# Kernel optimization log

Hardware: AMD Instinct MI355X
Metric: run time of the kernel (lower is better)

Reference implementation:

```python
import jax, jax.numpy as jnp
import numpy as np

N_HEAD = 8
LN_EPS = 1e-5


def layernorm(x, g, b):
    m = x.mean(-1, keepdims=True)
    var = x.var(-1, keepdims=True)
    return (x - m) / jnp.sqrt(var + LN_EPS) * g + b


def mha(xq, xkv, key_pad, w, b, wo, bo):
    # w: [3, D, D] (q,k,v proj), key_pad: [B, Nk] bool, True = ignore
    B, Nq, D = xq.shape
    H, dh = N_HEAD, D // N_HEAD
    q = (xq @ w[0] + b[0]).reshape(B, Nq, H, dh)
    k = (xkv @ w[1] + b[1]).reshape(B, -1, H, dh)
    v = (xkv @ w[2] + b[2]).reshape(B, -1, H, dh)
    s = jnp.einsum('bqhd,bkhd->bhqk', q, k) * (1.0 / np.float32(np.sqrt(dh)))
    s = jnp.where(key_pad[:, None, None, :], jnp.float32(-1e9), s)
    a = jax.nn.softmax(s, axis=-1)
    o = jnp.einsum('bhqk,bkhd->bqhd', a, v).reshape(B, Nq, D)
    return o @ wo + bo


def coattn_layer(v, q, v_pad, q_pad, aw, ab, awo, abo, lg, lb, fw1, fb1, fw2, fb2):
    # self-attention + residual + LN
    v_a = layernorm(v + mha(v, v, v_pad, aw[0], ab[0], awo[0], abo[0]), lg[0], lb[0])
    q_a = layernorm(q + mha(q, q, q_pad, aw[1], ab[1], awo[1], abo[1]), lg[1], lb[1])
    # cross attention: note qv_attn consumes OUTPUT of vq_attn (as in original)
    vq_out = mha(v_a, q_a, q_pad, aw[2], ab[2], awo[2], abo[2])
    qv_out = mha(q_a, vq_out, v_pad, aw[3], ab[3], awo[3], abo[3])
    v = layernorm(v + vq_out, lg[2], lb[2])
    q = layernorm(q + qv_out, lg[3], lb[3])
    # FFN (fc -> relu -> fc), residual + LN
    v = layernorm(v + (jax.nn.relu(v @ fw1[0] + fb1[0]) @ fw2[0] + fb2[0]), lg[4], lb[4])
    q = layernorm(q + (jax.nn.relu(q @ fw1[1] + fb1[1]) @ fw2[1] + fb2[1]), lg[5], lb[5])
    return v, q


def setup_inputs() -> dict:
    key = jax.random.key(0)
    B, NV, NQ, D, L = 8, 512, 512, 512, 4
    DF = 4 * D
    ks = jax.random.split(key, 12)
    sd = 0.02
    inp = {}
    inp['v'] = jax.random.normal(ks[0], (B, NV, D), jnp.float32)
    inp['q'] = jax.random.normal(ks[1], (B, NQ, D), jnp.float32)
    vm = jax.random.randint(ks[2], (B, NV), 0, 2, jnp.int32)
    qm = jax.random.randint(ks[3], (B, NQ), 0, 2, jnp.int32)
    inp['v_mask'] = vm.at[:, 0].set(1)  # ensure >=1 valid token per row
    inp['q_mask'] = qm.at[:, 0].set(1)
    inp['attn_w'] = sd * jax.random.normal(ks[4], (L, 4, 3, D, D), jnp.float32)
    inp['attn_b'] = jnp.zeros((L, 4, 3, D), jnp.float32)
    inp['attn_wo'] = sd * jax.random.normal(ks[5], (L, 4, D, D), jnp.float32)
    inp['attn_bo'] = jnp.zeros((L, 4, D), jnp.float32)
    inp['ln_g'] = jnp.ones((L, 6, D), jnp.float32)
    inp['ln_b'] = jnp.zeros((L, 6, D), jnp.float32)
    inp['ffn_w1'] = sd * jax.random.normal(ks[6], (L, 2, D, DF), jnp.float32)
    inp['ffn_b1'] = jnp.zeros((L, 2, DF), jnp.float32)
    inp['ffn_w2'] = sd * jax.random.normal(ks[7], (L, 2, DF, D), jnp.float32)
    inp['ffn_b2'] = jnp.zeros((L, 2, D), jnp.float32)
    inp['att_w'] = sd * jax.random.normal(ks[8], (D,), jnp.float32)
    inp['att_b'] = jnp.zeros((), jnp.float32)
    return inp


def reference(v, q, attn_w, attn_b, attn_wo, attn_bo, ln_g, ln_b,
              ffn_w1, ffn_b1, ffn_w2, ffn_b2, att_w, att_b, v_mask, q_mask):
    v_pad = v_mask == 0  # True = pad (original: ~v_mask.bool())
    q_pad = q_mask == 0
    L = attn_w.shape[0]
    for i in range(L):
        v, q = coattn_layer(v, q, v_pad, q_pad,
                            attn_w[i], attn_b[i], attn_wo[i], attn_bo[i],
                            ln_g[i], ln_b[i],
                            ffn_w1[i], ffn_b1[i], ffn_w2[i], ffn_b2[i])
    # att_net(v_i * q_j) is a bilinear form: sum_k v_bvk * q_bqk * w_k + bias
    s = jnp.einsum('bvk,bqk,k->bvq', v, q, att_w) + att_b
    cross_mask = v_pad[:, :, None] | q_pad[:, None, :]
    s = jnp.where(cross_mask, jnp.float32(-1e9), s)
    att_maps = jax.nn.softmax(s, axis=-1)
    v_num, q_num = v.shape[1], q.shape[1]
    seq_scale = 1.0 / np.float32(np.sqrt(v_num * q_num))
    return jnp.einsum('bvk,bvq,bqk->bk', v, att_maps, q) * seq_scale
```

## Files before the change

### kernel.cpp

```cpp
#include <hip/hip_runtime.h>
#include <hip/hip_bf16.h>

typedef __hip_bfloat16 bf16;
typedef __attribute__((ext_vector_type(8))) short short8;
typedef __attribute__((ext_vector_type(4))) short short4v;
typedef __attribute__((ext_vector_type(4))) float f32x4;

#define AS1 __attribute__((address_space(1)))
#define AS3 __attribute__((address_space(3)))

#define B_  8
#define N_  512
#define D_  512
#define H_  8
#define DH_ 64
#define DF_ 2048
#define L_  4

static __device__ __forceinline__ short bfbits(float x) {
  bf16 t = __float2bfloat16(x);
  return *reinterpret_cast<short*>(&t);
}

__global__ __launch_bounds__(256) void k_prep2(const float* __restrict__ a,
                                               float* __restrict__ fa, bf16* __restrict__ ba,
                                               const float* __restrict__ bsrc,
                                               float* __restrict__ fb, bf16* __restrict__ bb,
                                               int n4) {
  int g = blockIdx.x * 256 + threadIdx.x;
  const float* s; float* f; bf16* o; long idx;
  if (g < n4) { s = a;    f = fa; o = ba; idx = (long)g * 4; }
  else        { s = bsrc; f = fb; o = bb; idx = (long)(g - n4) * 4; }
  float4 v = *(const float4*)(s + idx);
  *(float4*)(f + idx) = v;
  bf16 ov[4] = { __float2bfloat16(v.x), __float2bfloat16(v.y),
                 __float2bfloat16(v.z), __float2bfloat16(v.w) };
  *(short4v*)&o[idx] = *(const short4v*)ov;
}

__global__ __launch_bounds__(256) void k_wt(const float* __restrict__ aw_l,
                                            const float* __restrict__ awo_l,
                                            const float* __restrict__ fw1_l,
                                            const float* __restrict__ fw2_l,
                                            bf16* __restrict__ WT)
{
  __shared__ float Ls[32][33];
  int bx = blockIdx.x;
  const float* src; bf16* dst; int R, C, tr, tc;
  if (bx < 4096) {
    int id = bx >> 8, t = bx & 255;
    int m = id >> 2, part = id & 3;
    src = (part < 3) ? (aw_l + ((long)m * 3 + part) * D_ * D_)
                     : (awo_l + (long)m * D_ * D_);
    dst = WT + (long)id * 262144; R = 512; C = 512; tr = t >> 4; tc = t & 15;
  } else if (bx < 6144) {
    int q = bx - 4096; int id = q >> 10; int t = q & 1023;
    src = fw1_l + (long)id * D_ * DF_; dst = WT + 4194304 + (long)id * 1048576;
    R = 512; C = 2048; tr = t >> 6; tc = t & 63;
  } else {
    int q = bx - 6144; int id = q >> 10; int t = q & 1023;
    src = fw2_l + (long)id * DF_ * D_; dst = WT + 6291456 + (long)id * 1048576;
    R = 2048; C = 512; tr = t >> 4; tc = t & 15;
  }
  int t = threadIdx.x;
  int lr = t >> 3, lc0 = (t & 7) * 4;
  float4 v = *(const float4*)(src + (long)(tr * 32 + lr) * C + tc * 32 + lc0);
  Ls[lr][lc0] = v.x; Ls[lr][lc0 + 1] = v.y; Ls[lr][lc0 + 2] = v.z; Ls[lr][lc0 + 3] = v.w;
  __syncthreads();
  bf16 ov[4];
#pragma unroll
  for (int j = 0; j < 4; ++j) ov[j] = __float2bfloat16(Ls[lc0 + j][lr]);
  *(short4v*)&dst[(long)(tc * 32 + lr) * R + tr * 32 + lc0] = *(const short4v*)ov;
}

template<int BN>
__global__ __launch_bounds__(256, 2) void k_mfma(
    const bf16* __restrict__ A, const bf16* __restrict__ A2,
    long aS, long aB, long aH, int lda,
    const bf16* __restrict__ Bm, long bS, long bB, long bH, int ldb,
    const float* __restrict__ bias, long biasS, float scale, int relu,
    float* __restrict__ Cf, long cfS, long cfB, long cfH, int ldcf,
    bf16* __restrict__ Cb, long cbS, long cbB, long cbH, int ldcb,
    int kLen, int Hh, int zPerS, int mode, int kSplit, long pStride)
{
  constexpr int MI = (BN == 128) ? 4 : 2;
  constexpr int NI = 4;
  __shared__ short As[2 * 128 * 32];
  __shared__ short Bs[2 * BN * 32];
  int tid = threadIdx.x;
  int w = tid >> 6, lane = tid & 63;
  int z = blockIdx.z;
  int kk = 0;
  if (kSplit > 1) { kk = z % kSplit; z /= kSplit; }
  int s = z / zPerS; int zz = z - s * zPerS;
  int zb = zz / Hh, zh = zz - zb * Hh;
  int row0 = blockIdx.y * 128;
  int col0 = blockIdx.x * BN;
  const bf16* Asel = (mode == 1 && col0 >= 512) ? A2 : A;
  const bf16* Ab = Asel + s * aS + zb * aB + zh * aH + (long)kk * kLen;
  const bf16* Bb = Bm + s * bS + zb * bB + zh * bH + (long)kk * kLen;
  int rw = (BN == 128) ? ((w >> 1) * 64) : (w * 32);
  int cw = (BN == 128) ? ((w & 1) * 64) : 0;
  int quad = lane >> 4, l16 = lane & 15;

  f32x4 acc[MI][NI];
#pragma unroll
  for (int i = 0; i < MI; ++i)
#pragma unroll
    for (int j = 0; j < NI; ++j) acc[i][j] = {0.f, 0.f, 0.f, 0.f};

  for (int k0 = 0; k0 < kLen; k0 += 64) {
#pragma unroll
    for (int hf = 0; hf < 2; ++hf) {
#pragma unroll
      for (int i = 0; i < 2; ++i) {
        int o = i * 4096 + w * 1024 + lane * 16;
        int r = o >> 6;
        const bf16* g = Ab + (long)(row0 + r) * lda + k0 + hf * 32 + ((o & 63) >> 1);
        char* lp = (char*)As + hf * 8192 + i * 4096 + w * 1024;
        __builtin_amdgcn_global_load_lds((const AS1 void*)g, (AS3 void*)lp, 16, 0, 0);
      }
      constexpr int BI = (BN == 128) ? 2 : 1;
#pragma unroll
      for (int i = 0; i < BI; ++i) {
        int o = i * 4096 + w * 1024 + lane * 16;
        int r = o >> 6;
        const bf16* g = Bb + (long)(col0 + r) * ldb + k0 + hf * 32 + ((o & 63) >> 1);
        char* lp = (char*)Bs + hf * (BN * 64) + i * 4096 + w * 1024;
        __builtin_amdgcn_global_load_lds((const AS1 void*)g, (AS3 void*)lp, 16, 0, 0);
      }
    }
    __syncthreads();
#pragma unroll
    for (int hf = 0; hf < 2; ++hf) {
      short8 af[MI], bfr[NI];
#pragma unroll
      for (int mi = 0; mi < MI; ++mi)
        af[mi] = *(const short8*)&As[hf * 4096 + (rw + mi * 16 + l16) * 32 + quad * 8];
#pragma unroll
      for (int ni = 0; ni < NI; ++ni)
        bfr[ni] = *(const short8*)&Bs[hf * (BN * 32) + (cw + ni * 16 + l16) * 32 + quad * 8];
#pragma unroll
      for (int mi = 0; mi < MI; ++mi)
#pragma unroll
        for (int ni = 0; ni < NI; ++ni)
          acc[mi][ni] = __builtin_amdgcn_mfma_f32_16x16x32_bf16(af[mi], bfr[ni], acc[mi][ni], 0, 0, 0);
    }
    __syncthreads();
  }

  const float* bp = (bias && kk == 0) ? bias + s * biasS : nullptr;
#pragma unroll
  for (int mi = 0; mi < MI; ++mi)
#pragma unroll
    for (int ni = 0; ni < NI; ++ni) {
      int cg = col0 + cw + ni * 16 + l16;
      float bv = bp ? bp[cg] : 0.0f;
#pragma unroll
      for (int r = 0; r < 4; ++r) {
        int rg = row0 + rw + mi * 16 + quad * 4 + r;
        float v = acc[mi][ni][r] * scale + bv;
        if (relu) v = fmaxf(v, 0.0f);
        if (mode == 1) {
          bf16* base = Cb + s * cbS;
          if (cg < 512) base[(long)rg * 512 + cg] = __float2bfloat16(v);
          else if (cg < 1024) base[2097152 + (long)rg * 512 + (cg - 512)] = __float2bfloat16(v);
          else {
            int c2 = cg - 1024;
            base[4194304 + ((long)((rg >> 9) * 8 + (c2 >> 6)) * 64 + (c2 & 63)) * 512 + (rg & 511)]
                = __float2bfloat16(v);
          }
        } else {
          if (Cf) Cf[s * cfS + (long)kk * pStride + zb * cfB + zh * cfH + (long)rg * ldcf + cg] = v;
          if (Cb) Cb[s * cbS + zb * cbB + zh * cbH + (long)rg * ldcb + cg] = __float2bfloat16(v);
        }
      }
    }
}

__global__ __launch_bounds__(256, 2) void k_flash(
    const bf16* __restrict__ QKV, long sStride,
    const int* __restrict__ km0, const int* __restrict__ km1, float scale)
{
  __shared__ short Ks[2 * 128 * 32];
  __shared__ short Vs[4 * 64 * 32];
  __shared__ short Ps[4 * 64 * 32];
  int tid = threadIdx.x, w = tid >> 6, lane = tid & 63;
  int quad = lane >> 4, l16 = lane & 15;
  int s = blockIdx.z;
  const bf16* base = QKV + s * sStride;
  int bh = blockIdx.y, b = bh >> 3, h = bh & 7;
  int qt = blockIdx.x;
  const int* km = (s ? km1 : km0) + (b << 9);
  const bf16* Kg = base + 2097152;
  const bf16* Vt = base + 4194304;
  bf16* Og = (bf16*)base;

  int qrow = (b << 9) + (qt << 6) + (w << 4) + l16;
  short8 qf[2];
  qf[0] = *(const short8*)&base[(long)qrow * 512 + h * 64 + quad * 8];
  qf[1] = *(const short8*)&base[(long)qrow * 512 + h * 64 + 32 + quad * 8];

  float m_[4], l_[4];
  f32x4 acc_o[4];
#pragma unroll
  for (int r = 0; r < 4; ++r) { m_[r] = -3e38f; l_[r] = 0.f; }
#pragma unroll
  for (int ni = 0; ni < 4; ++ni) acc_o[ni] = {0.f, 0.f, 0.f, 0.f};

  for (int kt = 0; kt < 4; ++kt) {
    __syncthreads();
#pragma unroll
    for (int i = 0; i < 4; ++i) {
      int o = i * 4096 + w * 1024 + lane * 16;
      int kc = o >> 13, rem = o & 8191;
      int n = rem >> 6, cb = rem & 63;
      const bf16* g = Kg + ((long)((b << 9) + kt * 128 + n) << 9) + h * 64 + kc * 32 + (cb >> 1);
      char* lp = (char*)Ks + i * 4096 + w * 1024;
      __builtin_amdgcn_global_load_lds((const AS1 void*)g, (AS3 void*)lp, 16, 0, 0);
    }
#pragma unroll
    for (int i = 0; i < 4; ++i) {
      int o = i * 4096 + w * 1024 + lane * 16;
      int kc = o >> 12, rem = o & 4095;
      int d = rem >> 6, cb = rem & 63;
      const bf16* g = Vt + ((long)((bh << 6) + d) << 9) + kt * 128 + kc * 32 + (cb >> 1);
      char* lp = (char*)Vs + i * 4096 + w * 1024;
      __builtin_amdgcn_global_load_lds((const AS1 void*)g, (AS3 void*)lp, 16, 0, 0);
    }
    __syncthreads();
    f32x4 sa[8];
#pragma unroll
    for (int ni = 0; ni < 8; ++ni) sa[ni] = {0.f, 0.f, 0.f, 0.f};
    __builtin_amdgcn_s_setprio(1);
#pragma unroll
    for (int kc = 0; kc < 2; ++kc)
#pragma unroll
      for (int ni = 0; ni < 8; ++ni) {
        short8 bfrag = *(const short8*)&Ks[kc * 4096 + (ni * 16 + l16) * 32 + quad * 8];
        sa[ni] = __builtin_amdgcn_mfma_f32_16x16x32_bf16(qf[kc], bfrag, sa[ni], 0, 0, 0);
      }
    __builtin_amdgcn_s_setprio(0);
    float sv[8][4];
#pragma unroll
    for (int ni = 0; ni < 8; ++ni) {
      int kmv = km[kt * 128 + ni * 16 + l16];
#pragma unroll
      for (int r = 0; r < 4; ++r)
        sv[ni][r] = kmv ? sa[ni][r] * scale : -1e9f;
    }
#pragma unroll
    for (int r = 0; r < 4; ++r) {
      float rmax = sv[0][r];
#pragma unroll
      for (int ni = 1; ni < 8; ++ni) rmax = fmaxf(rmax, sv[ni][r]);
#pragma unroll
      for (int o = 1; o < 16; o <<= 1) rmax = fmaxf(rmax, __shfl_xor(rmax, o, 64));
      float newm = fmaxf(m_[r], rmax);
      float alpha = __expf(m_[r] - newm);
      float psum = 0.f;
#pragma unroll
      for (int ni = 0; ni < 8; ++ni) {
        float p = __expf(sv[ni][r] - newm);
        sv[ni][r] = p; psum += p;
      }
#pragma unroll
      for (int o = 1; o < 16; o <<= 1) psum += __shfl_xor(psum, o, 64);
      l_[r] = l_[r] * alpha + psum;
      m_[r] = newm;
#pragma unroll
      for (int ni = 0; ni < 4; ++ni) acc_o[ni][r] *= alpha;
    }
#pragma unroll
    for (int ni = 0; ni < 8; ++ni) {
      int j = ni * 16 + l16;
      short* pp = &Ps[(j >> 5) * 2048 + (w * 16 + quad * 4) * 32 + (j & 31)];
#pragma unroll
      for (int r = 0; r < 4; ++r) pp[r * 32] = bfbits(sv[ni][r]);
    }
    __builtin_amdgcn_s_setprio(1);
#pragma unroll
    for (int kcp = 0; kcp < 4; ++kcp) {
      short8 af = *(const short8*)&Ps[kcp * 2048 + (w * 16 + l16) * 32 + quad * 8];
#pragma unroll
      for (int ni = 0; ni < 4; ++ni) {
        short8 bfrag = *(const short8*)&Vs[kcp * 2048 + (ni * 16 + l16) * 32 + quad * 8];
        acc_o[ni] = __builtin_amdgcn_mfma_f32_16x16x32_bf16(af, bfrag, acc_o[ni], 0, 0, 0);
      }
    }
    __builtin_amdgcn_s_setprio(0);
  }
  float linv[4];
#pragma unroll
  for (int r = 0; r < 4; ++r) linv[r] = 1.0f / l_[r];
#pragma unroll
  for (int ni = 0; ni < 4; ++ni)
#pragma unroll
    for (int r = 0; r < 4; ++r) {
      long row = (b << 9) + (qt << 6) + (w << 4) + quad * 4 + r;
      Og[row * 512 + h * 64 + ni * 16 + l16] = __float2bfloat16(acc_o[ni][r] * linv[r]);
    }
}

__global__ __launch_bounds__(256) void k_ln2(
    const float* x0, const float* g0, const float* b0, float* yf0, bf16* yb0,
    const float* x1, const float* g1, const float* b1, float* yf1, bf16* yb1,
    const float* __restrict__ P, long pstr)
{
  int t = threadIdx.x;
  int rh = t >> 7;
  long row = (long)blockIdx.x * 2 + rh;
  int sel = row >= 4096;
  long r = row & 4095;
  const float* x  = sel ? x1 : x0;
  const float* g  = sel ? g1 : g0;
  const float* bb = sel ? b1 : b0;
  float* yf = sel ? yf1 : yf0;
  bf16*  yb = sel ? yb1 : yb0;
  int c = (t & 127) * 4;
  const float* xr = x + r * D_ + c;
  const float* ra = P + (sel ? 2 : 0) * pstr + r * D_ + c;
  const float* rb = ra + pstr;
  float4 xv = *(const float4*)xr;
  float4 av = *(const float4*)ra;
  float4 bv = *(const float4*)rb;
  float4 v = { xv.x + av.x + bv.x, xv.y + av.y + bv.y,
               xv.z + av.z + bv.z, xv.w + av.w + bv.w };
  float s  = v.x + v.y + v.z + v.w;
  float ss = v.x * v.x + v.y * v.y + v.z * v.z + v.w * v.w;
#pragma unroll
  for (int o = 32; o > 0; o >>= 1) {
    s  += __shfl_down(s, o, 64);
    ss += __shfl_down(ss, o, 64);
  }
  __shared__ float rs[4];
  __shared__ float rss[4];
  int lane = t & 63, wid = t >> 6;
  if (lane == 0) { rs[wid] = s; rss[wid] = ss; }
  __syncthreads();
  s  = rs[rh * 2]  + rs[rh * 2 + 1];
  ss = rss[rh * 2] + rss[rh * 2 + 1];
  float mean = s * (1.0f / D_);
  float var = ss * (1.0f / D_) - mean * mean;
  float rstd = rsqrtf(var + 1e-5f);
  float4 gg = *(const float4*)(g + c);
  float4 b4 = *(const float4*)(bb + c);
  float4 o4 = { (v.x - mean) * rstd * gg.x + b4.x,
                (v.y - mean) * rstd * gg.y + b4.y,
                (v.z - mean) * rstd * gg.z + b4.z,
                (v.w - mean) * rstd * gg.w + b4.w };
  if (yf) *(float4*)(yf + r * D_ + c) = o4;
  if (yb) {
    bf16 ov[4] = { __float2bfloat16(o4.x), __float2bfloat16(o4.y),
                   __float2bfloat16(o4.z), __float2bfloat16(o4.w) };
    *(short4v*)&yb[r * D_ + c] = *(const short4v*)ov;
  }
}

__global__ __launch_bounds__(256) void k_sum2bf(const float* __restrict__ a,
                                                const float* __restrict__ b,
                                                bf16* __restrict__ o)
{
  int i = (blockIdx.x * 256 + threadIdx.x) * 4;
  float4 va = *(const float4*)(a + i);
  float4 vb = *(const float4*)(b + i);
  bf16 ov[4] = { __float2bfloat16(va.x + vb.x), __float2bfloat16(va.y + vb.y),
                 __float2bfloat16(va.z + vb.z), __float2bfloat16(va.w + vb.w) };
  *(short4v*)&o[i] = *(const short4v*)ov;
}

__global__ __launch_bounds__(256) void k_softmax_x(float* __restrict__ S,
                                                   const int* __restrict__ vm,
                                                   const int* __restrict__ qm)
{
  int wrow = blockIdx.x * 4 + (threadIdx.x >> 6);
  int lane = threadIdx.x & 63;
  int b = wrow >> 9, i = wrow & 511;
  bool rowpad = (vm[(b << 9) + i] == 0);
  float* p = S + (long)wrow * 512;
  const int* qb = qm + (b << 9);
  int j0 = lane * 8;
  float4 a0 = *(const float4*)(p + j0);
  float4 a1 = *(const float4*)(p + j0 + 4);
  int4 m0 = *(const int4*)(qb + j0);
  int4 m1 = *(const int4*)(qb + j0 + 4);
  float v[8];
  v[0] = (rowpad || !m0.x) ? -1e9f : a0.x; v[1] = (rowpad || !m0.y) ? -1e9f : a0.y;
  v[2] = (rowpad || !m0.z) ? -1e9f : a0.z; v[3] = (rowpad || !m0.w) ? -1e9f : a0.w;
  v[4] = (rowpad || !m1.x) ? -1e9f : a1.x; v[5] = (rowpad || !m1.y) ? -1e9f : a1.y;
  v[6] = (rowpad || !m1.z) ? -1e9f : a1.z; v[7] = (rowpad || !m1.w) ? -1e9f : a1.w;
  float mx = v[0];
#pragma unroll
  for (int u = 1; u < 8; ++u) mx = fmaxf(mx, v[u]);
#pragma unroll
  for (int o = 1; o < 64; o <<= 1) mx = fmaxf(mx, __shfl_xor(mx, o, 64));
  float e[8], sum = 0.f;
#pragma unroll
  for (int u = 0; u < 8; ++u) { e[u] = __expf(v[u] - mx); sum += e[u]; }
#pragma unroll
  for (int o = 1; o < 64; o <<= 1) sum += __shfl_xor(sum, o, 64);
  float inv = 1.0f / sum;
  bf16 ob[8];
#pragma unroll
  for (int u = 0; u < 8; ++u) ob[u] = __float2bfloat16(e[u] * inv);
  bf16* pb = (bf16*)p;
  *(short8*)&pb[j0] = *(const short8*)ob;
}

__global__ __launch_bounds__(256) void k_vwqt(const float* __restrict__ V,
                                              const float* __restrict__ Q,
                                              const float* __restrict__ w,
                                              bf16* __restrict__ Vw, bf16* __restrict__ Qt)
{
  __shared__ float Ls[32][33];
  int bx = blockIdx.x, t = threadIdx.x;
  if (bx < 2048) {
    int i = bx * 1024 + t * 4;
    float4 v = *(const float4*)(V + i);
    int k = i & 511;
    bf16 o[4] = { __float2bfloat16(v.x * w[k]),     __float2bfloat16(v.y * w[k + 1]),
                  __float2bfloat16(v.z * w[k + 2]), __float2bfloat16(v.w * w[k + 3]) };
    *(short4v*)&Vw[i] = *(const short4v*)o;
  } else {
    int q = bx - 2048; int b = q >> 8; int tq = q & 255;
    int tr = tq >> 4, tc = tq & 15;
    const float* Qb = Q + (long)b * 262144;
    bf16* Qtb = Qt + (long)b * 262144;
    int lr = t >> 3, lc0 = (t & 7) * 4;
    float4 v = *(const float4*)(Qb + (long)(tr * 32 + lr) * 512 + tc * 32 + lc0);
    Ls[lr][lc0] = v.x; Ls[lr][lc0 + 1] = v.y; Ls[lr][lc0 + 2] = v.z; Ls[lr][lc0 + 3] = v.w;
    __syncthreads();
    bf16 ov[4];
#pragma unroll
    for (int j = 0; j < 4; ++j) ov[j] = __float2bfloat16(Ls[lc0 + j][lr]);
    *(short4v*)&Qtb[(long)(tc * 32 + lr) * 512 + tr * 32 + lc0] = *(const short4v*)ov;
  }
}

__global__ __launch_bounds__(256) void k_final_part(
    const float* __restrict__ V, const float* __restrict__ QT, float* __restrict__ Pf)
{
  int bx = blockIdx.x;
  int b = bx >> 5, rem = bx & 31;
  int kc = rem >> 4, is = rem & 15;
  int k = (kc << 8) + threadIdx.x;
  const float* Vb = V  + (long)b * N_ * D_ + (long)(is * 32) * D_ + k;
  const float* Tb = QT + (long)b * N_ * D_ + (long)(is * 32) * D_ + k;
  float acc = 0.0f;
#pragma unroll 8
  for (int i = 0; i < 32; ++i) acc += Vb[(long)i * D_] * Tb[(long)i * D_];
  Pf[bx * 256 + threadIdx.x] = acc;
}

__global__ __launch_bounds__(256) void k_fred(const float* __restrict__ Pf,
                                              float* __restrict__ out)
{
  int b = blockIdx.x >> 1, kc = blockIdx.x & 1;
  int k = (kc << 8) + threadIdx.x;
  float s = 0.0f;
#pragma unroll
  for (int is = 0; is < 16; ++is)
    s += Pf[(((b << 5) | (kc << 4) | is) << 8) + threadIdx.x];
  out[b * D_ + k] = s * (1.0f / 512.0f);
}

extern "C" void kernel_launch(void* const* d_in, const int* in_sizes, int n_in,
                              void* d_out, int out_size, void* d_ws, size_t ws_size,
                              hipStream_t stream)
{
  const float* in_v   = (const float*)d_in[0];
  const float* in_q   = (const float*)d_in[1];
  const int*   v_mask = (const int*)  d_in[2];
  const int*   q_mask = (const int*)  d_in[3];
  const float* aw  = (const float*)d_in[4];
  const float* ab  = (const float*)d_in[5];
  const float* awo = (const float*)d_in[6];
  const float* abo = (const float*)d_in[7];
  const float* lg  = (const float*)d_in[8];
  const float* lb  = (const float*)d_in[9];
  const float* fw1 = (const float*)d_in[10];
  const float* fb1 = (const float*)d_in[11];
  const float* fw2 = (const float*)d_in[12];
  const float* fb2 = (const float*)d_in[13];
  const float* atw = (const float*)d_in[14];
  const float* atb = (const float*)d_in[15];
  float* out = (float*)d_out;
  (void)atb;

  const int SZ = B_ * N_ * D_;
  char* wsb = (char*)d_ws;
  const long MB = 1024L * 1024;
  float* Vcur   = (float*)(wsb + 0 * MB);
  float* Qcur   = (float*)(wsb + 8 * MB);
  float* P0     = (float*)(wsb + 16 * MB);
  const long PSZ = 2097152;
  bf16*  WT     = (bf16*) (wsb + 48 * MB);
  bf16*  Vcur_b = (bf16*) (wsb + 64 * MB);
  bf16*  Qcur_b = (bf16*) (wsb + 68 * MB);
  bf16*  VA_b   = (bf16*) (wsb + 72 * MB);
  bf16*  QA_b   = (bf16*) (wsb + 76 * MB);
  bf16*  VQ_b   = (bf16*) (wsb + 80 * MB);
  bf16*  QKV0   = (bf16*) (wsb + 84 * MB);
  bf16*  Hid    = (bf16*) (wsb + 108 * MB);
  float* Sf     = P0;
  bf16*  Vw_b   = (bf16*) (wsb + 24 * MB);
  bf16*  Qt_b   = (bf16*) (wsb + 28 * MB);
  float* Tfin   = (float*)(wsb + 32 * MB);
  float* Pf     = (float*)(wsb + 41 * MB);

  const long ZBIG = 1000000;

  k_prep2<<<4096, 256, 0, stream>>>(in_v, Vcur, Vcur_b, in_q, Qcur, Qcur_b, SZ / 4);

  for (int l = 0; l < L_; ++l) {
    const float* lgl = lg + (long)l * 6 * D_;
    const float* lbl = lb + (long)l * 6 * D_;
    k_wt<<<8192, 256, 0, stream>>>(aw + (long)l * 12 * 262144,
                                   awo + (long)l * 4 * 262144,
                                   fw1 + (long)l * 2 * 1048576,
                                   fw2 + (long)l * 2 * 1048576, WT);
    k_mfma<128><<<dim3(12, 32, 2), 256, 0, stream>>>(
        Vcur_b, Vcur_b, 2097152, 0, 0, 512,
        WT, 1048576, 0, 0, 512,
        ab + (long)l * 4 * 1536, 1536, 1.f, 0,
        nullptr, 0, 0, 0, 0, QKV0, 6291456, 0, 0, 0,
        512, 1, 1, 1, 1, 0);
    k_flash<<<dim3(8, 64, 2), 256, 0, stream>>>(QKV0, 6291456, v_mask, q_mask, 0.125f);
    k_mfma<128><<<dim3(4, 32, 4), 256, 0, stream>>>(
        QKV0, QKV0, 6291456, 0, 0, 512,
        WT + 3 * 262144, 1048576, 0, 0, 512,
        abo + (long)l * 4 * 512, 512, 1.f, 0,
        P0, 2 * PSZ, 0, 0, 512, nullptr, 0, 0, 0, 0,
        256, 1, 1, 0, 2, PSZ);
    k_ln2<<<4096, 256, 0, stream>>>(Vcur, lgl + 0 * D_, lbl + 0 * D_, nullptr, VA_b,
                                    Qcur, lgl + 1 * D_, lbl + 1 * D_, nullptr, QA_b,
                                    P0, PSZ);
    k_mfma<128><<<dim3(12, 32, 1), 256, 0, stream>>>(
        VA_b, QA_b, 0, 0, 0, 512,
        WT + 2 * 1048576, 0, 0, 0, 512,
        ab + (long)(l * 4 + 2) * 1536, 0, 1.f, 0,
        nullptr, 0, 0, 0, 0, QKV0, 0, 0, 0, 0,
        512, 1, 1, 1, 1, 0);
    k_flash<<<dim3(8, 64, 1), 256, 0, stream>>>(QKV0, 0, q_mask, q_mask, 0.125f);
    k_mfma<64><<<dim3(8, 32, 2), 256, 0, stream>>>(
        QKV0, QKV0, 0, 0, 0, 512,
        WT + (2 * 4 + 3) * 262144, 0, 0, 0, 512,
        abo + (long)(l * 4 + 2) * 512, 0, 1.f, 0,
        P0, 0, 0, 0, 512, nullptr, 0, 0, 0, 0,
        256, 1, 1, 0, 2, PSZ);
    k_sum2bf<<<2048, 256, 0, stream>>>(P0, P0 + PSZ, VQ_b);
    k_mfma<128><<<dim3(12, 32, 1), 256, 0, stream>>>(
        QA_b, VQ_b, 0, 0, 0, 512,
        WT + 3 * 1048576, 0, 0, 0, 512,
        ab + (long)(l * 4 + 3) * 1536, 0, 1.f, 0,
        nullptr, 0, 0, 0, 0, QKV0, 0, 0, 0, 0,
        512, 1, 1, 1, 1, 0);
    k_flash<<<dim3(8, 64, 1), 256, 0, stream>>>(QKV0, 0, v_mask, v_mask, 0.125f);
    k_mfma<64><<<dim3(8, 32, 2), 256, 0, stream>>>(
        QKV0, QKV0, 0, 0, 0, 512,
        WT + (3 * 4 + 3) * 262144, 0, 0, 0, 512,
        abo + (long)(l * 4 + 3) * 512, 0, 1.f, 0,
        P0 + 2 * PSZ, 0, 0, 0, 512, nullptr, 0, 0, 0, 0,
        256, 1, 1, 0, 2, PSZ);
    k_ln2<<<4096, 256, 0, stream>>>(Vcur, lgl + 2 * D_, lbl + 2 * D_, Vcur, Vcur_b,
                                    Qcur, lgl + 3 * D_, lbl + 3 * D_, Qcur, Qcur_b,
                                    P0, PSZ);
    k_mfma<128><<<dim3(16, 32, 2), 256, 0, stream>>>(
        Vcur_b, Vcur_b, 2097152, 0, 0, 512,
        WT + 4194304, 1048576, 0, 0, 512,
        fb1 + (long)l * 2 * 2048, 2048, 1.f, 1,
        nullptr, 0, 0, 0, 0, Hid, 8388608, 0, 0, 2048,
        512, 1, 1, 0, 1, 0);
    k_mfma<128><<<dim3(4, 32, 4), 256, 0, stream>>>(
        Hid, Hid, 8388608, 0, 0, 2048,
        WT + 6291456, 1048576, 0, 0, 2048,
        fb2 + (long)l * 2 * 512, 512, 1.f, 0,
        P0, 2 * PSZ, 0, 0, 512, nullptr, 0, 0, 0, 0,
        1024, 1, 1, 0, 2, PSZ);
    k_ln2<<<4096, 256, 0, stream>>>(Vcur, lgl + 4 * D_, lbl + 4 * D_, Vcur, Vcur_b,
                                    Qcur, lgl + 5 * D_, lbl + 5 * D_, Qcur, Qcur_b,
                                    P0, PSZ);
  }

  k_vwqt<<<4096, 256, 0, stream>>>(Vcur, Qcur, atw, Vw_b, Qt_b);
  k_mfma<128><<<dim3(4, 4, 8), 256, 0, stream>>>(
      Vw_b, Vw_b, 0, 262144, 0, 512, Qcur_b, 0, 262144, 0, 512,
      nullptr, 0, 1.f, 0,
      Sf, 0, 262144, 0, 512, nullptr, 0, 0, 0, 0,
      512, 1, ZBIG, 0, 1, 0);
  k_softmax_x<<<1024, 256, 0, stream>>>(Sf, v_mask, q_mask);
  k_mfma<128><<<dim3(4, 4, 8), 256, 0, stream>>>(
      (const bf16*)Sf, (const bf16*)Sf, 0, 524288, 0, 1024, Qt_b, 0, 262144, 0, 512,
      nullptr, 0, 1.f, 0,
      Tfin, 0, 262144, 0, 512, nullptr, 0, 0, 0, 0,
      512, 1, ZBIG, 0, 1, 0);
  k_final_part<<<256, 256, 0, stream>>>(Vcur, Tfin, Pf);
  k_fred<<<16, 256, 0, stream>>>(Pf, out);

  (void)in_sizes; (void)n_in; (void)out_size; (void)ws_size;
}
```

Before: 1.447 ms.

## Rewrite flash attention with register-resident 32x32 MFMA and transposed S

Replaces the LDS-staged 16x16x32 flash attention with a version that loads K and V fragments straight from global memory into registers. It computes S transposed with 32x32x16 MFMAs so each lane owns one query row, and passes P to the PV MFMA through cross-lane shuffles instead of LDS. It also uses an exp2 softmax with the scale folded in, a ballot-based key mask, and 128 query rows per block, which halves the grid. This drops LDS traffic and barriers, but every wave reloads K and V from global memory or L2 without block-level sharing, and register pressure rises.

After: 1.466 ms. Within noise of the previous version (+1.4%).

```diff
diff --git a/kernel.cpp b/kernel.cpp
--- a/kernel.cpp
+++ b/kernel.cpp
@@ -5,6 +5,8 @@
 typedef __attribute__((ext_vector_type(8))) short short8;
 typedef __attribute__((ext_vector_type(4))) short short4v;
 typedef __attribute__((ext_vector_type(4))) float f32x4;
+typedef __attribute__((ext_vector_type(16))) float f32x16;
+typedef __attribute__((ext_vector_type(4))) unsigned int uint4v;
 
 #define AS1 __attribute__((address_space(1)))
 #define AS3 __attribute__((address_space(3)))
@@ -17,9 +19,11 @@
 #define DF_ 2048
 #define L_  4
 
-static __device__ __forceinline__ short bfbits(float x) {
-  bf16 t = __float2bfloat16(x);
-  return *reinterpret_cast<short*>(&t);
+static __device__ __forceinline__ unsigned packbf2(float lo, float hi) {
+  bf16 a = __float2bfloat16(lo), b = __float2bfloat16(hi);
+  unsigned short ua = *reinterpret_cast<unsigned short*>(&a);
+  unsigned short ub = *reinterpret_cast<unsigned short*>(&b);
+  return (unsigned)ua | ((unsigned)ub << 16);
 }
 
 __global__ __launch_bounds__(256) void k_prep2(const float* __restrict__ a,
@@ -182,11 +186,8 @@
     const bf16* __restrict__ QKV, long sStride,
     const int* __restrict__ km0, const int* __restrict__ km1, float scale)
 {
-  __shared__ short Ks[2 * 128 * 32];
-  __shared__ short Vs[4 * 64 * 32];
-  __shared__ short Ps[4 * 64 * 32];
   int tid = threadIdx.x, w = tid >> 6, lane = tid & 63;
-  int quad = lane >> 4, l16 = lane & 15;
+  int l31 = lane & 31, hi = lane >> 5;
   int s = blockIdx.z;
   const bf16* base = QKV + s * sStride;
   int bh = blockIdx.y, b = bh >> 3, h = bh & 7;
@@ -196,109 +197,120 @@
   const bf16* Vt = base + 4194304;
   bf16* Og = (bf16*)base;
 
-  int qrow = (b << 9) + (qt << 6) + (w << 4) + l16;
-  short8 qf[2];
-  qf[0] = *(const short8*)&base[(long)qrow * 512 + h * 64 + quad * 8];
-  qf[1] = *(const short8*)&base[(long)qrow * 512 + h * 64 + 32 + quad * 8];
-
-  float m_[4], l_[4];
-  f32x4 acc_o[4];
-#pragma unroll
-  for (int r = 0; r < 4; ++r) { m_[r] = -3e38f; l_[r] = 0.f; }
-#pragma unroll
-  for (int ni = 0; ni < 4; ++ni) acc_o[ni] = {0.f, 0.f, 0.f, 0.f};
-
-  for (int kt = 0; kt < 4; ++kt) {
-    __syncthreads();
-#pragma unroll
-    for (int i = 0; i < 4; ++i) {
-      int o = i * 4096 + w * 1024 + lane * 16;
-      int kc = o >> 13, rem = o & 8191;
-      int n = rem >> 6, cb = rem & 63;
-      const bf16* g = Kg + ((long)((b << 9) + kt * 128 + n) << 9) + h * 64 + kc * 32 + (cb >> 1);
-      char* lp = (char*)Ks + i * 4096 + w * 1024;
-      __builtin_amdgcn_global_load_lds((const AS1 void*)g, (AS3 void*)lp, 16, 0, 0);
-    }
-#pragma unroll
-    for (int i = 0; i < 4; ++i) {
-      int o = i * 4096 + w * 1024 + lane * 16;
-      int kc = o >> 12, rem = o & 4095;
-      int d = rem >> 6, cb = rem & 63;
-      const bf16* g = Vt + ((long)((bh << 6) + d) << 9) + kt * 128 + kc * 32 + (cb >> 1);
-      char* lp = (char*)Vs + i * 4096 + w * 1024;
-      __builtin_amdgcn_global_load_lds((const AS1 void*)g, (AS3 void*)lp, 16, 0, 0);
-    }
-    __syncthreads();
-    f32x4 sa[8];
-#pragma unroll
-    for (int ni = 0; ni < 8; ++ni) sa[ni] = {0.f, 0.f, 0.f, 0.f};
+  long qrow = (b << 9) + (qt << 7) + (w << 5) + l31;
+  const bf16* Qp = base + qrow * 512 + h * 64 + hi * 8;
+  short8 qf[4];
+#pragma unroll
+  for (int c = 0; c < 4; ++c) qf[c] = *(const short8*)(Qp + c * 16);
+
+  float m_ = -3e38f, l_ = 0.f;
+  f32x16 acc0, acc1;
+#pragma unroll
+  for (int r = 0; r < 16; ++r) { acc0[r] = 0.f; acc1[r] = 0.f; }
+
+  const float cl2 = scale * 1.44269504f;
+  const bf16* Kb = Kg + (((long)(b << 9)) << 9) + h * 64 + hi * 8;
+  const bf16* Vb = Vt + (((long)(bh << 6)) << 9) + hi * 8;
+
+  for (int kt = 0; kt < 8; ++kt) {
+    short8 kf0[4], kf1[4];
+#pragma unroll
+    for (int c = 0; c < 4; ++c) {
+      kf0[c] = *(const short8*)(Kb + (((long)(kt * 64 + l31)) << 9) + c * 16);
+      kf1[c] = *(const short8*)(Kb + (((long)(kt * 64 + 32 + l31)) << 9) + c * 16);
+    }
+    short8 vf0[4], vf1[4];
+#pragma unroll
+    for (int c = 0; c < 4; ++c) {
+      vf0[c] = *(const short8*)(Vb + (((long)l31) << 9) + kt * 64 + c * 16);
+      vf1[c] = *(const short8*)(Vb + (((long)(32 + l31)) << 9) + kt * 64 + c * 16);
+    }
+    unsigned long long mwall = __ballot(km[kt * 64 + lane] != 0);
+    unsigned mlo  = ((unsigned)mwall) >> (4 * hi);
+    unsigned mhi2 = ((unsigned)(mwall >> 32)) >> (4 * hi);
+
+    f32x16 sa0, sa1;
+#pragma unroll
+    for (int r = 0; r < 16; ++r) { sa0[r] = 0.f; sa1[r] = 0.f; }
     __builtin_amdgcn_s_setprio(1);
 #pragma unroll
-    for (int kc = 0; kc < 2; ++kc)
-#pragma unroll
-      for (int ni = 0; ni < 8; ++ni) {
-        short8 bfrag = *(const short8*)&Ks[kc * 4096 + (ni * 16 + l16) * 32 + quad * 8];
-        sa[ni] = __builtin_amdgcn_mfma_f32_16x16x32_bf16(qf[kc], bfrag, sa[ni], 0, 0, 0);
+    for (int c = 0; c < 4; ++c) {
+      sa0 = __builtin_amdgcn_mfma_f32_32x32x16_bf16(kf0[c], qf[c], sa0, 0, 0, 0);
+      sa1 = __builtin_amdgcn_mfma_f32_32x32x16_bf16(kf1[c], qf[c], sa1, 0, 0, 0);
+    }
+    __builtin_amdgcn_s_setprio(0);
+
+    float t[16];
+#pragma unroll
+    for (int r = 0; r < 16; ++r) t[r] = fmaxf(sa0[r], sa1[r]);
+#pragma unroll
+    for (int st = 8; st > 0; st >>= 1)
+#pragma unroll
+      for (int r = 0; r < st; ++r) t[r] = fmaxf(t[r], t[r + st]);
+    float mx = fmaxf(t[0], __shfl_xor(t[0], 32, 64));
+    float newm = fmaxf(m_, mx);
+    float al = exp2f((m_ - newm) * cl2);
+    m_ = newm;
+
+    float ps = 0.f;
+    unsigned fw[4][4];
+#pragma unroll
+    for (int g = 0; g < 4; ++g) {
+      unsigned mword = (g < 2) ? mlo : mhi2;
+      int g2 = g & 1;
+      float p[8];
+#pragma unroll
+      for (int j = 0; j < 8; ++j) {
+        float sv = (g < 2) ? ((g2 == 0) ? sa0[j] : sa0[8 + j])
+                           : ((g2 == 0) ? sa1[j] : sa1[8 + j]);
+        float e = exp2f((sv - newm) * cl2);
+        int sh = (j & 3) + 8 * (j >> 2) + 16 * g2;
+        p[j] = ((mword >> sh) & 1u) ? e : 0.f;
+        ps += p[j];
       }
-    __builtin_amdgcn_s_setprio(0);
-    float sv[8][4];
-#pragma unroll
-    for (int ni = 0; ni < 8; ++ni) {
-      int kmv = km[kt * 128 + ni * 16 + l16];
-#pragma unroll
-      for (int r = 0; r < 4; ++r)
-        sv[ni][r] = kmv ? sa[ni][r] * scale : -1e9f;
-    }
-#pragma unroll
-    for (int r = 0; r < 4; ++r) {
-      float rmax = sv[0][r];
-#pragma unroll
-      for (int ni = 1; ni < 8; ++ni) rmax = fmaxf(rmax, sv[ni][r]);
-#pragma unroll
-      for (int o = 1; o < 16; o <<= 1) rmax = fmaxf(rmax, __shfl_xor(rmax, o, 64));
-      float newm = fmaxf(m_[r], rmax);
-      float alpha = __expf(m_[r] - newm);
-      float psum = 0.f;
-#pragma unroll
-      for (int ni = 0; ni < 8; ++ni) {
-        float p = __expf(sv[ni][r] - newm);
-        sv[ni][r] = p; psum += p;
-      }
-#pragma unroll
-      for (int o = 1; o < 16; o <<= 1) psum += __shfl_xor(psum, o, 64);
-      l_[r] = l_[r] * alpha + psum;
-      m_[r] = newm;
-#pragma unroll
-      for (int ni = 0; ni < 4; ++ni) acc_o[ni][r] *= alpha;
-    }
-#pragma unroll
-    for (int ni = 0; ni < 8; ++ni) {
-      int j = ni * 16 + l16;
-      short* pp = &Ps[(j >> 5) * 2048 + (w * 16 + quad * 4) * 32 + (j & 31)];
-#pragma unroll
-      for (int r = 0; r < 4; ++r) pp[r * 32] = bfbits(sv[ni][r]);
-    }
+      unsigned A = packbf2(p[0], p[1]);
+      unsigned Bw = packbf2(p[2], p[3]);
+      unsigned C = packbf2(p[4], p[5]);
+      unsigned Dw = packbf2(p[6], p[7]);
+      unsigned pA = (unsigned)__shfl_xor((int)A, 32, 64);
+      unsigned pB = (unsigned)__shfl_xor((int)Bw, 32, 64);
+      unsigned pC = (unsigned)__shfl_xor((int)C, 32, 64);
+      unsigned pD = (unsigned)__shfl_xor((int)Dw, 32, 64);
+      fw[g][0] = hi ? pC : A;
+      fw[g][1] = hi ? pD : Bw;
+      fw[g][2] = hi ? C : pA;
+      fw[g][3] = hi ? Dw : pB;
+    }
+    ps += __shfl_xor(ps, 32, 64);
+    l_ = l_ * al + ps;
+
+#pragma unroll
+    for (int r = 0; r < 16; ++r) { acc0[r] *= al; acc1[r] *= al; }
+
     __builtin_amdgcn_s_setprio(1);
 #pragma unroll
-    for (int kcp = 0; kcp < 4; ++kcp) {
-      short8 af = *(const short8*)&Ps[kcp * 2048 + (w * 16 + l16) * 32 + quad * 8];
-#pragma unroll
-      for (int ni = 0; ni < 4; ++ni) {
-        short8 bfrag = *(const short8*)&Vs[kcp * 2048 + (ni * 16 + l16) * 32 + quad * 8];
-        acc_o[ni] = __builtin_amdgcn_mfma_f32_16x16x32_bf16(af, bfrag, acc_o[ni], 0, 0, 0);
-      }
+    for (int g = 0; g < 4; ++g) {
+      uint4v tw = { fw[g][0], fw[g][1], fw[g][2], fw[g][3] };
+      short8 pf = *reinterpret_cast<short8*>(&tw);
+      acc0 = __builtin_amdgcn_mfma_f32_32x32x16_bf16(vf0[g], pf, acc0, 0, 0, 0);
+      acc1 = __builtin_amdgcn_mfma_f32_32x32x16_bf16(vf1[g], pf, acc1, 0, 0, 0);
     }
     __builtin_amdgcn_s_setprio(0);
   }
-  float linv[4];
-#pragma unroll
-  for (int r = 0; r < 4; ++r) linv[r] = 1.0f / l_[r];
-#pragma unroll
-  for (int ni = 0; ni < 4; ++ni)
-#pragma unroll
-    for (int r = 0; r < 4; ++r) {
-      long row = (b << 9) + (qt << 6) + (w << 4) + quad * 4 + r;
-      Og[row * 512 + h * 64 + ni * 16 + l16] = __float2bfloat16(acc_o[ni][r] * linv[r]);
+
+  float linv = 1.0f / l_;
+#pragma unroll
+  for (int dc = 0; dc < 2; ++dc)
+#pragma unroll
+    for (int g = 0; g < 4; ++g) {
+      int d0 = dc * 32 + 8 * g + 4 * hi;
+      bf16 o[4];
+#pragma unroll
+      for (int rr = 0; rr < 4; ++rr) {
+        float av = dc ? acc1[g * 4 + rr] : acc0[g * 4 + rr];
+        o[rr] = __float2bfloat16(av * linv);
+      }
+      *(short4v*)&Og[qrow * 512 + h * 64 + d0] = *(const short4v*)o;
     }
 }
 
@@ -525,7 +537,7 @@
         ab + (long)l * 4 * 1536, 1536, 1.f, 0,
         nullptr, 0, 0, 0, 0, QKV0, 6291456, 0, 0, 0,
         512, 1, 1, 1, 1, 0);
-    k_flash<<<dim3(8, 64, 2), 256, 0, stream>>>(QKV0, 6291456, v_mask, q_mask, 0.125f);
+    k_flash<<<dim3(4, 64, 2), 256, 0, stream>>>(QKV0, 6291456, v_mask, q_mask, 0.125f);
     k_mfma<128><<<dim3(4, 32, 4), 256, 0, stream>>>(
         QKV0, QKV0, 6291456, 0, 0, 512,
         WT + 3 * 262144, 1048576, 0, 0, 512,
@@ -541,7 +553,7 @@
         ab + (long)(l * 4 + 2) * 1536, 0, 1.f, 0,
         nullptr, 0, 0, 0, 0, QKV0, 0, 0, 0, 0,
         512, 1, 1, 1, 1, 0);
-    k_flash<<<dim3(8, 64, 1), 256, 0, stream>>>(QKV0, 0, q_mask, q_mask, 0.125f);
+    k_flash<<<dim3(4, 64, 1), 256, 0, stream>>>(QKV0, 0, q_mask, q_mask, 0.125f);
     k_mfma<64><<<dim3(8, 32, 2), 256, 0, stream>>>(
         QKV0, QKV0, 0, 0, 0, 512,
         WT + (2 * 4 + 3) * 262144, 0, 0, 0, 512,
@@ -555,7 +567,7 @@
         ab + (long)(l * 4 + 3) * 1536, 0, 1.f, 0,
         nullptr, 0, 0, 0, 0, QKV0, 0, 0, 0, 0,
         512, 1, 1, 1, 1, 0);
-    k_flash<<<dim3(8, 64, 1), 256, 0, stream>>>(QKV0, 0, v_mask, v_mask, 0.125f);
+    k_flash<<<dim3(4, 64, 1), 256, 0, stream>>>(QKV0, 0, v_mask, v_mask, 0.125f);
     k_mfma<64><<<dim3(8, 32, 2), 256, 0, stream>>>(
         QKV0, QKV0, 0, 0, 0, 512,
         WT + (3 * 4 + 3) * 262144, 0, 0, 0, 512,
```
